# Kernel optimization log

Measured on AMD Instinct MI355X. Metric: run time of the kernel, lower is better.

Reference implementation:

```python
import jax, jax.numpy as jnp
import numpy as np

BETA = 1.0  # init kwarg beta


def setup_inputs() -> dict:
    key = jax.random.key(0)
    k1, k2 = jax.random.split(key)
    B, K = 8192, 64
    policy_logps = jax.random.normal(k1, (B, K), dtype=jnp.float32)
    reward_scores = jax.random.uniform(k2, (B, K), dtype=jnp.float32)
    return {"policy_logps": policy_logps, "reward_scores": reward_scores}


def reference(policy_logps, reward_scores):
    B, K = policy_logps.shape
    s = policy_logps  # rf_free=True -> scores = policy_logps
    r = reward_scores

    # ranks: 1-based rank of each item when rewards sorted descending
    order = jnp.argsort(-r, axis=-1)              # [B, K]
    ranks = jnp.argsort(order, axis=-1) + 1        # [B, K]
    inv_discount = 1.0 / jnp.log1p(ranks.astype(s.dtype))  # [B, K]
    gain = 2.0 * r - 1.0                            # [B, K]

    # pairwise matrices [B, K, K]; loop in original covers i > j (strict lower triangle)
    delta = jnp.abs(gain[:, :, None] - gain[:, None, :]) * \
            jnp.abs(inv_discount[:, :, None] - inv_discount[:, None, :])
    diff = s[:, :, None] - s[:, None, :]
    term = delta * jax.nn.log_sigmoid(-BETA * diff)

    mask = jnp.tril(jnp.ones((K, K), dtype=bool), k=-1)  # i > j
    loss_sum = jnp.sum(jnp.where(mask[None], term, 0.0))
    count = B * (K * (K - 1) // 2)
    return -loss_sum / count
```

## Files before the change

kernel.cpp:

```cpp
#include <hip/hip_runtime.h>

#define KDIM 64
#define WAVES_PER_BLOCK 4
#define ROWS_PER_WAVE 2
#define ROWS_PER_BLOCK (WAVES_PER_BLOCK * ROWS_PER_WAVE)

__global__ __launch_bounds__(256) void rankdpo_main(
    const float* __restrict__ s_in, const float* __restrict__ r_in,
    float* __restrict__ partials, int B)
{
    const int wave = threadIdx.x >> 6;
    const int lane = threadIdx.x & 63;
    const int row0 = blockIdx.x * ROWS_PER_BLOCK + wave * ROWS_PER_WAVE;
    const int row1 = row0 + 1;
    const int a0 = (row0 < B ? row0 : 0) * KDIM + lane;
    const int a1 = (row1 < B ? row1 : 0) * KDIM + lane;

    const float s0 = s_in[a0], r0 = r_in[a0];
    const float s1 = s_in[a1], r1 = r_in[a1];

    int c0 = 0, c1 = 0;
    #pragma unroll
    for (int j = 0; j < KDIM; ++j) {
        float rj0 = __uint_as_float(__builtin_amdgcn_readlane(__float_as_uint(r0), j));
        float rj1 = __uint_as_float(__builtin_amdgcn_readlane(__float_as_uint(r1), j));
        c0 += (rj0 > r0) || (rj0 == r0 && j < lane);
        c1 += (rj1 > r1) || (rj1 == r1 && j < lane);
    }
    const float invd0 = __builtin_amdgcn_rcpf(
        0.69314718056f * __builtin_amdgcn_logf((float)(c0 + 2)));
    const float invd1 = __builtin_amdgcn_rcpf(
        0.69314718056f * __builtin_amdgcn_logf((float)(c1 + 2)));
    const float g0 = 2.0f * r0 - 1.0f;
    const float g1 = 2.0f * r1 - 1.0f;

    float p0 = 0.0f, p1 = 0.0f;
    #pragma unroll
    for (int d = 1; d <= 32; ++d) {
        const int pj = (lane - d) & 63;
        float sj0 = __shfl(s0, pj), gj0 = __shfl(g0, pj), dj0 = __shfl(invd0, pj);
        float sj1 = __shfl(s1, pj), gj1 = __shfl(g1, pj), dj1 = __shfl(invd1, pj);

        float del0 = fabsf(g0 - gj0) * fabsf(invd0 - dj0);
        float del1 = fabsf(g1 - gj1) * fabsf(invd1 - dj1);
        if (d == 32 && lane < 32) { del0 = 0.0f; del1 = 0.0f; }

        float u0 = (lane >= d) ? (s0 - sj0) : (sj0 - s0);
        float u1 = (lane >= d) ? (s1 - sj1) : (sj1 - s1);

        float e0 = __builtin_amdgcn_exp2f(-1.44269504089f * fabsf(u0));
        float e1 = __builtin_amdgcn_exp2f(-1.44269504089f * fabsf(u1));
        float sp0 = fmaxf(u0, 0.0f) + 0.69314718056f * __builtin_amdgcn_logf(1.0f + e0);
        float sp1 = fmaxf(u1, 0.0f) + 0.69314718056f * __builtin_amdgcn_logf(1.0f + e1);

        p0 = fmaf(del0, sp0, p0);
        p1 = fmaf(del1, sp1, p1);
    }
    if (row0 >= B) p0 = 0.0f;
    if (row1 >= B) p1 = 0.0f;

    float pacc = p0 + p1;
    #pragma unroll
    for (int off = 32; off > 0; off >>= 1)
        pacc += __shfl_down(pacc, off);

    __shared__ float wsum[WAVES_PER_BLOCK];
    if (lane == 0) wsum[wave] = pacc;
    __syncthreads();
    if (threadIdx.x == 0)
        partials[blockIdx.x] = wsum[0] + wsum[1] + wsum[2] + wsum[3];
}

__global__ __launch_bounds__(256) void rankdpo_reduce(
    const float* __restrict__ partials, int n, float* __restrict__ out,
    double inv_count)
{
    double sum = 0.0;
    for (int i = threadIdx.x; i < n; i += 256)
        sum += (double)partials[i];
    __shared__ double sh[256];
    sh[threadIdx.x] = sum;
    __syncthreads();
    for (int st = 128; st > 0; st >>= 1) {
        if (threadIdx.x < st) sh[threadIdx.x] += sh[threadIdx.x + st];
        __syncthreads();
    }
    if (threadIdx.x == 0)
        out[0] = (float)(sh[0] * inv_count);
}

extern "C" void kernel_launch(void* const* d_in, const int* in_sizes, int n_in,
                              void* d_out, int out_size, void* d_ws, size_t ws_size,
                              hipStream_t stream) {
    const float* s = (const float*)d_in[0];
    const float* r = (const float*)d_in[1];
    float* out = (float*)d_out;

    const int BK = in_sizes[0];
    const int B  = BK / KDIM;
    const int nblocks = (B + ROWS_PER_BLOCK - 1) / ROWS_PER_BLOCK;

    float* partials = (float*)d_ws;

    const long long count = (long long)B * (KDIM * (KDIM - 1) / 2);
    const double inv_count = 1.0 / (double)count;

    rankdpo_main<<<nblocks, 256, 0, stream>>>(s, r, partials, B);
    rankdpo_reduce<<<1, 256, 0, stream>>>(partials, nblocks, out, inv_count);
}
```

Baseline: 72.04 us.

## Fuse final reduction via atomics and streamline rank and softplus math

Drops the second reduce kernel: each block scales its sum and atomically adds it into the output, which is zeroed by a memset first. The rank count now uses one 64-bit key comparison that packs the reward bits with the inverted lane index, in place of separate greater and equal tests. Softplus drops the max/abs stable form and computes log2(1+exp2(±x·log2e)) directly, folding the ln2 factors into the loss scale. Neighbour exchange uses explicit ds_bpermute, and float atomics make the sum order nondeterministic; the unstable softplus could overflow for large score gaps.

After: 76.25 us. 5.8% more time.

```diff
diff --git a/kernel.cpp b/kernel.cpp
--- a/kernel.cpp
+++ b/kernel.cpp
@@ -7,7 +7,7 @@
 
 __global__ __launch_bounds__(256) void rankdpo_main(
     const float* __restrict__ s_in, const float* __restrict__ r_in,
-    float* __restrict__ partials, int B)
+    float* __restrict__ out, int B, float inv_count)
 {
     const int wave = threadIdx.x >> 6;
     const int lane = threadIdx.x & 63;
@@ -19,42 +19,49 @@
     const float s0 = s_in[a0], r0 = r_in[a0];
     const float s1 = s_in[a1], r1 = r_in[a1];
 
+    const unsigned long long k0 =
+        ((unsigned long long)__float_as_uint(r0) << 32) | (unsigned int)(~lane);
+    const unsigned long long k1 =
+        ((unsigned long long)__float_as_uint(r1) << 32) | (unsigned int)(~lane);
     int c0 = 0, c1 = 0;
     #pragma unroll
     for (int j = 0; j < KDIM; ++j) {
-        float rj0 = __uint_as_float(__builtin_amdgcn_readlane(__float_as_uint(r0), j));
-        float rj1 = __uint_as_float(__builtin_amdgcn_readlane(__float_as_uint(r1), j));
-        c0 += (rj0 > r0) || (rj0 == r0 && j < lane);
-        c1 += (rj1 > r1) || (rj1 == r1 && j < lane);
+        unsigned int rb0 = (unsigned int)__builtin_amdgcn_readlane(__float_as_int(r0), j);
+        unsigned int rb1 = (unsigned int)__builtin_amdgcn_readlane(__float_as_int(r1), j);
+        unsigned long long kj0 = ((unsigned long long)rb0 << 32) | (unsigned int)(~j);
+        unsigned long long kj1 = ((unsigned long long)rb1 << 32) | (unsigned int)(~j);
+        c0 += (kj0 > k0);
+        c1 += (kj1 > k1);
     }
-    const float invd0 = __builtin_amdgcn_rcpf(
-        0.69314718056f * __builtin_amdgcn_logf((float)(c0 + 2)));
-    const float invd1 = __builtin_amdgcn_rcpf(
-        0.69314718056f * __builtin_amdgcn_logf((float)(c1 + 2)));
+    const float invd0 = __builtin_amdgcn_rcpf(__builtin_amdgcn_logf((float)(c0 + 2)));
+    const float invd1 = __builtin_amdgcn_rcpf(__builtin_amdgcn_logf((float)(c1 + 2)));
     const float g0 = 2.0f * r0 - 1.0f;
     const float g1 = 2.0f * r1 - 1.0f;
 
+    const float LOG2E = 1.44269504088896f;
+    const int laneb = lane << 2;
     float p0 = 0.0f, p1 = 0.0f;
     #pragma unroll
     for (int d = 1; d <= 32; ++d) {
-        const int pj = (lane - d) & 63;
-        float sj0 = __shfl(s0, pj), gj0 = __shfl(g0, pj), dj0 = __shfl(invd0, pj);
-        float sj1 = __shfl(s1, pj), gj1 = __shfl(g1, pj), dj1 = __shfl(invd1, pj);
+        const int addr = (laneb - (d << 2)) & 255;
+        float sj0 = __int_as_float(__builtin_amdgcn_ds_bpermute(addr, __float_as_int(s0)));
+        float gj0 = __int_as_float(__builtin_amdgcn_ds_bpermute(addr, __float_as_int(g0)));
+        float dj0 = __int_as_float(__builtin_amdgcn_ds_bpermute(addr, __float_as_int(invd0)));
+        float sj1 = __int_as_float(__builtin_amdgcn_ds_bpermute(addr, __float_as_int(s1)));
+        float gj1 = __int_as_float(__builtin_amdgcn_ds_bpermute(addr, __float_as_int(g1)));
+        float dj1 = __int_as_float(__builtin_amdgcn_ds_bpermute(addr, __float_as_int(invd1)));
+
+        const float qc = (lane >= d) ? LOG2E : -LOG2E;
 
         float del0 = fabsf(g0 - gj0) * fabsf(invd0 - dj0);
         float del1 = fabsf(g1 - gj1) * fabsf(invd1 - dj1);
         if (d == 32 && lane < 32) { del0 = 0.0f; del1 = 0.0f; }
 
-        float u0 = (lane >= d) ? (s0 - sj0) : (sj0 - s0);
-        float u1 = (lane >= d) ? (s1 - sj1) : (sj1 - s1);
+        float l0 = __builtin_amdgcn_logf(1.0f + __builtin_amdgcn_exp2f(qc * (s0 - sj0)));
+        float l1 = __builtin_amdgcn_logf(1.0f + __builtin_amdgcn_exp2f(qc * (s1 - sj1)));
 
-        float e0 = __builtin_amdgcn_exp2f(-1.44269504089f * fabsf(u0));
-        float e1 = __builtin_amdgcn_exp2f(-1.44269504089f * fabsf(u1));
-        float sp0 = fmaxf(u0, 0.0f) + 0.69314718056f * __builtin_amdgcn_logf(1.0f + e0);
-        float sp1 = fmaxf(u1, 0.0f) + 0.69314718056f * __builtin_amdgcn_logf(1.0f + e1);
-
-        p0 = fmaf(del0, sp0, p0);
-        p1 = fmaf(del1, sp1, p1);
+        p0 = fmaf(del0, l0, p0);
+        p1 = fmaf(del1, l1, p1);
     }
     if (row0 >= B) p0 = 0.0f;
     if (row1 >= B) p1 = 0.0f;
@@ -67,26 +74,10 @@
     __shared__ float wsum[WAVES_PER_BLOCK];
     if (lane == 0) wsum[wave] = pacc;
     __syncthreads();
-    if (threadIdx.x == 0)
-        partials[blockIdx.x] = wsum[0] + wsum[1] + wsum[2] + wsum[3];
-}
-
-__global__ __launch_bounds__(256) void rankdpo_reduce(
-    const float* __restrict__ partials, int n, float* __restrict__ out,
-    double inv_count)
-{
-    double sum = 0.0;
-    for (int i = threadIdx.x; i < n; i += 256)
-        sum += (double)partials[i];
-    __shared__ double sh[256];
-    sh[threadIdx.x] = sum;
-    __syncthreads();
-    for (int st = 128; st > 0; st >>= 1) {
-        if (threadIdx.x < st) sh[threadIdx.x] += sh[threadIdx.x + st];
-        __syncthreads();
+    if (threadIdx.x == 0) {
+        float bsum = wsum[0] + wsum[1] + wsum[2] + wsum[3];
+        atomicAdd(out, bsum * inv_count);
     }
-    if (threadIdx.x == 0)
-        out[0] = (float)(sh[0] * inv_count);
 }
 
 extern "C" void kernel_launch(void* const* d_in, const int* in_sizes, int n_in,
@@ -100,11 +91,9 @@
     const int B  = BK / KDIM;
     const int nblocks = (B + ROWS_PER_BLOCK - 1) / ROWS_PER_BLOCK;
 
-    float* partials = (float*)d_ws;
+    const long long count = (long long)B * (KDIM * (KDIM - 1) / 2);
+    const float inv_count = (float)(1.0 / (double)count);
 
-    const long long count = (long long)B * (KDIM * (KDIM - 1) / 2);
-    const double inv_count = 1.0 / (double)count;
-
-    rankdpo_main<<<nblocks, 256, 0, stream>>>(s, r, partials, B);
-    rankdpo_reduce<<<1, 256, 0, stream>>>(partials, nblocks, out, inv_count);
+    hipMemsetAsync(d_out, 0, sizeof(float), stream);
+    rankdpo_main<<<nblocks, 256, 0, stream>>>(s, r, out, B, inv_count);
 }
```
